# Performance work log

Measured on AMD Instinct MI355X. Metric: run time of the kernel, lower is better.

Reference implementation:

```python
import jax, jax.numpy as jnp
import numpy as np

B, LI, LT = 1, 2048, 256
HID, HEADS, HD = 3072, 24, 128
MLP = 4 * HID  # 12288
EPS = 1e-6


def setup_inputs() -> dict:
    key = jax.random.key(0)
    ks = jax.random.split(key, 12)
    n = lambda k, s, sc=1.0: jax.random.normal(k, s, dtype=jnp.float32) * sc
    # RoPE tables, interleaved-pair layout over head_dim
    theta = 10000.0 ** (-jnp.arange(0, HD, 2, dtype=jnp.float32) / HD)  # [HD/2]
    ang = jnp.arange(LI, dtype=jnp.float32)[:, None] * theta[None, :]   # [LI, HD/2]
    freqs_cos = jnp.repeat(jnp.cos(ang), 2, axis=-1)  # [LI, HD]
    freqs_sin = jnp.repeat(jnp.sin(ang), 2, axis=-1)
    return {
        "img": n(ks[0], (B, LI, HID)),
        "txt": n(ks[1], (B, LT, HID)),
        "vec": n(ks[2], (B, HID)),
        "freqs_cos": freqs_cos,
        "freqs_sin": freqs_sin,
        "w1": n(ks[3], (3 * HID + MLP, HID), 0.02),
        "b1": jnp.zeros((3 * HID + MLP,), jnp.float32),
        "w2": n(ks[4], (HID, HID + MLP), 0.02),
        "b2": jnp.zeros((HID,), jnp.float32),
        "q_norm_w": jnp.ones((HD,), jnp.float32),
        "k_norm_w": jnp.ones((HD,), jnp.float32),
        "mod_w": n(ks[5], (3 * HID, HID), 0.02),
        "mod_b": jnp.zeros((3 * HID,), jnp.float32),
        "txt_len": LT,
    }


def _layernorm(x):  # no affine, eps=1e-6
    mu = x.mean(-1, keepdims=True)
    var = ((x - mu) ** 2).mean(-1, keepdims=True)
    return (x - mu) * jax.lax.rsqrt(var + EPS)


def _rmsnorm(x, w):  # per-head-dim RMSNorm with affine weight
    ms = (x * x).mean(-1, keepdims=True)
    return x * jax.lax.rsqrt(ms + EPS) * w


def _rope(x, cos, sin):  # x: [B,L,H,D]; interleaved complex rotation
    xr = x.reshape(*x.shape[:-1], HD // 2, 2)
    rot = jnp.stack([-xr[..., 1], xr[..., 0]], axis=-1).reshape(x.shape)
    return x * cos[None, :, None, :] + rot * sin[None, :, None, :]


def reference(img, txt, vec, freqs_cos, freqs_sin, w1, b1, w2, b2,
              q_norm_w, k_norm_w, mod_w, mod_b, txt_len):
    H = img.shape[-1]
    Li = img.shape[1]
    # modulation: SiLU(vec) @ W -> shift, scale, gate
    mod = jax.nn.silu(vec) @ mod_w.T + mod_b           # [B, 3H]
    shift, scale, gate = jnp.split(mod, 3, axis=-1)
    modulate = lambda x: x * (1.0 + scale[:, None, :]) + shift[:, None, :]
    img_mod = modulate(_layernorm(img))
    txt_mod = modulate(_layernorm(txt))
    x_mod = jnp.concatenate([img_mod, txt_mod], axis=1)  # [B,S,H]
    Bb, S = x_mod.shape[0], x_mod.shape[1]
    # fused QKV projection (slices of linear1)
    qkv = x_mod @ w1[: 3 * H].T + b1[: 3 * H]
    q, k, v = [t.reshape(Bb, S, HEADS, HD) for t in jnp.split(qkv, 3, axis=-1)]
    q = _rmsnorm(q, q_norm_w)
    k = _rmsnorm(k, k_norm_w)
    # RoPE only on the img portion of the sequence
    q = jnp.concatenate([_rope(q[:, :Li], freqs_cos, freqs_sin), q[:, Li:]], axis=1)
    k = jnp.concatenate([_rope(k[:, :Li], freqs_cos, freqs_sin), k[:, Li:]], axis=1)
    # full (non-causal) attention over img+txt tokens
    logits = jnp.einsum('bqhd,bkhd->bhqk', q, k) * (HD ** -0.5)
    probs = jax.nn.softmax(logits, axis=-1)
    attn = jnp.einsum('bhqk,bkhd->bqhd', probs, v).reshape(Bb, S, H)
    # MLP branch (linear1 mlp slice) with gelu-tanh, then fused linear2
    mlp = jax.nn.gelu(x_mod @ w1[3 * H:].T + b1[3 * H:], approximate=True)
    out = jnp.concatenate([attn, mlp], axis=-1) @ w2.T + b2  # [B,S,H]
    img_out = img + gate[:, None, :] * out[:, :-txt_len]
    txt_out = txt + gate[:, None, :] * out[:, -txt_len:]
    return img_out, txt_out
```

## Files before the change

kernel.cpp:

```cpp
#include <hip/hip_runtime.h>
#include <hip/hip_bf16.h>

#define DI __device__ __forceinline__

typedef __attribute__((ext_vector_type(8))) short bf8;
typedef __attribute__((ext_vector_type(4))) float f4;
typedef __attribute__((ext_vector_type(8))) unsigned short us8;

#define LI    2048
#define LT    256
#define SEQ   2304
#define HID   3072
#define NHEAD 24
#define HD    128
#define N1    21504
#define QKVW  9216
#define N2CAT 15360

DI unsigned short f2bf(float f) {
  union { float f; unsigned u; } v; v.f = f;
  unsigned r = v.u + 0x7FFFu + ((v.u >> 16) & 1u);
  return (unsigned short)(r >> 16);
}
DI float bf2f(unsigned short h) {
  union { unsigned u; float f; } v; v.u = ((unsigned)h) << 16;
  return v.f;
}

DI void gload16(const void* g, void* l) {
  __builtin_amdgcn_global_load_lds(
      (const __attribute__((address_space(1))) void*)g,
      (__attribute__((address_space(3))) void*)l, 16, 0, 0);
}

DI f4 mfma16(bf8 a, bf8 b, f4 c) {
  return __builtin_amdgcn_mfma_f32_16x16x32_bf16(a, b, c, 0, 0, 0);
}

__global__ void k_mod(const float* __restrict__ vec, const float* __restrict__ mw,
                      const float* __restrict__ mb, float* __restrict__ mod) {
  int row = blockIdx.x * 4 + (threadIdx.x >> 6);
  int lane = threadIdx.x & 63;
  const float4* wr = (const float4*)(mw + (size_t)row * HID);
  const float4* vv = (const float4*)vec;
  float s = 0.f;
  for (int i = lane; i < HID / 4; i += 64) {
    float4 w4 = wr[i], x4 = vv[i];
    s += (x4.x / (1.f + __expf(-x4.x))) * w4.x;
    s += (x4.y / (1.f + __expf(-x4.y))) * w4.y;
    s += (x4.z / (1.f + __expf(-x4.z))) * w4.z;
    s += (x4.w / (1.f + __expf(-x4.w))) * w4.w;
  }
#pragma unroll
  for (int m = 32; m; m >>= 1) s += __shfl_xor(s, m);
  if (lane == 0) mod[row] = s + mb[row];
}

__global__ void k_lnmod(const float* __restrict__ img, const float* __restrict__ txt,
                        const float* __restrict__ mod, unsigned short* __restrict__ xmod) {
  int t = blockIdx.x;
  const float* x = (t < LI) ? (img + (size_t)t * HID) : (txt + (size_t)(t - LI) * HID);
  const float4* x4 = (const float4*)x;
  float4 v[3];
  float s = 0.f, ss = 0.f;
#pragma unroll
  for (int j = 0; j < 3; ++j) {
    v[j] = x4[threadIdx.x + j * 256];
    s  += v[j].x + v[j].y + v[j].z + v[j].w;
    ss += v[j].x * v[j].x + v[j].y * v[j].y + v[j].z * v[j].z + v[j].w * v[j].w;
  }
#pragma unroll
  for (int m = 32; m; m >>= 1) { s += __shfl_xor(s, m); ss += __shfl_xor(ss, m); }
  __shared__ float red[8];
  int wv = threadIdx.x >> 6;
  if ((threadIdx.x & 63) == 0) { red[wv] = s; red[4 + wv] = ss; }
  __syncthreads();
  s = red[0] + red[1] + red[2] + red[3];
  ss = red[4] + red[5] + red[6] + red[7];
  float mu = s * (1.f / HID);
  float var = ss * (1.f / HID) - mu * mu;
  float inv = rsqrtf(var + 1e-6f);
  const float* shift = mod;
  const float* scale = mod + HID;
#pragma unroll
  for (int j = 0; j < 3; ++j) {
    int i = threadIdx.x + j * 256;
    int c = i * 4;
    ushort4 o;
    o.x = f2bf((v[j].x - mu) * inv * (1.f + scale[c + 0]) + shift[c + 0]);
    o.y = f2bf((v[j].y - mu) * inv * (1.f + scale[c + 1]) + shift[c + 1]);
    o.z = f2bf((v[j].z - mu) * inv * (1.f + scale[c + 2]) + shift[c + 2]);
    o.w = f2bf((v[j].w - mu) * inv * (1.f + scale[c + 3]) + shift[c + 3]);
    ((ushort4*)xmod)[(size_t)t * (HID / 4) + i] = o;
  }
}

__global__ void k_f2bf(const float* __restrict__ in, unsigned short* __restrict__ out, int n4) {
  int stride = gridDim.x * blockDim.x;
  for (int i = blockIdx.x * blockDim.x + threadIdx.x; i < n4; i += stride) {
    float4 f = ((const float4*)in)[i];
    ushort4 o;
    o.x = f2bf(f.x); o.y = f2bf(f.y); o.z = f2bf(f.z); o.w = f2bf(f.w);
    ((ushort4*)out)[i] = o;
  }
}

#define BAR()    asm volatile("s_barrier" ::: "memory")
#define VMCNT6() asm volatile("s_waitcnt vmcnt(6)" ::: "memory")
#define LGKM0()  do { asm volatile("s_waitcnt lgkmcnt(0)" ::: "memory"); \
                      __builtin_amdgcn_sched_barrier(0); } while (0)

__global__ __launch_bounds__(512, 2) void k_gemm1(const unsigned short* __restrict__ xmod,
    const unsigned short* __restrict__ w1b, const float* __restrict__ b1,
    unsigned short* __restrict__ qkv, unsigned short* __restrict__ amlp) {
  __shared__ unsigned short As[2][256 * 64];
  __shared__ unsigned short Bs[2][256 * 64];
  const int K = HID;
  const int NT = K / 64;
  int tid = threadIdx.x, lane = tid & 63, wid = tid >> 6;
  int wr = wid >> 2, wc = wid & 3;

  int b = blockIdx.x;
  const int Q = 756 / 8, R = 756 % 8;
  int xcd = b & 7, idx = b >> 3;
  int wg = (xcd < R ? xcd * (Q + 1) : R * (Q + 1) + (xcd - R) * Q) + idx;
  int bm = wg % 9, bn = wg / 9;

  const unsigned short* Ag = xmod + (size_t)bm * 256 * K;
  const unsigned short* Bg = w1b + (size_t)bn * 256 * K;

  int sgran = (lane & 7) ^ ((lane >> 3) & 7);
  int srow = wid * 16 + (lane >> 3);

#define STAGE_A(bufi, t, hh) do { \
    gload16(Ag + (size_t)((hh)*128 + srow) * K + (t)*64 + sgran*8, \
            &As[bufi][((hh)*128 + wid*16) * 64]); \
    gload16(Ag + (size_t)((hh)*128 + 8 + srow) * K + (t)*64 + sgran*8, \
            &As[bufi][((hh)*128 + wid*16 + 8) * 64]); \
  } while (0)
#define STAGE_B(bufi, t, hh) do { \
    gload16(Bg + (size_t)((hh)*128 + srow) * K + (t)*64 + sgran*8, \
            &Bs[bufi][((hh)*128 + wid*16) * 64]); \
    gload16(Bg + (size_t)((hh)*128 + 8 + srow) * K + (t)*64 + sgran*8, \
            &Bs[bufi][((hh)*128 + wid*16 + 8) * 64]); \
  } while (0)

  int rA = wr * 128 + (lane & 15);
  int rB = wc * 64 + (lane & 15);
  int qq = lane >> 4, l7 = lane & 7;

  f4 acc[8][4];
#pragma unroll
  for (int m = 0; m < 8; ++m)
#pragma unroll
    for (int n = 0; n < 4; ++n) acc[m][n] = (f4){0.f, 0.f, 0.f, 0.f};
  bf8 a[8][2], bfr[4][2];

#define LOADFRAGS(bufi) do { \
    _Pragma("unroll") for (int m = 0; m < 8; ++m) \
      _Pragma("unroll") for (int s = 0; s < 2; ++s) \
        a[m][s] = *(const bf8*)&As[bufi][(rA + m*16)*64 + (((s*4 + qq) ^ l7) << 3)]; \
    _Pragma("unroll") for (int n = 0; n < 4; ++n) \
      _Pragma("unroll") for (int s = 0; s < 2; ++s) \
        bfr[n][s] = *(const bf8*)&Bs[bufi][(rB + n*16)*64 + (((s*4 + qq) ^ l7) << 3)]; \
  } while (0)

#define QUAD(mh, nh) do { \
    __builtin_amdgcn_s_setprio(1); \
    _Pragma("unroll") for (int m = 4*(mh); m < 4*(mh)+4; ++m) \
      _Pragma("unroll") for (int n = 2*(nh); n < 2*(nh)+2; ++n) \
        _Pragma("unroll") for (int s = 0; s < 2; ++s) \
          acc[m][n] = mfma16(a[m][s], bfr[n][s], acc[m][n]); \
    __builtin_amdgcn_s_setprio(0); \
  } while (0)

  STAGE_A(0, 0, 0); STAGE_A(0, 0, 1); STAGE_B(0, 0, 0); STAGE_B(0, 0, 1);
  STAGE_A(1, 1, 0); STAGE_A(1, 1, 1); STAGE_B(1, 1, 0);
  VMCNT6();
  BAR();

  for (int i = 0; i < NT / 2; ++i) {
    int t1 = 2 * i + 1;
    int t2 = 2 * i + 2; if (t2 > NT - 1) t2 = NT - 1;
    int t3 = 2 * i + 3; if (t3 > NT - 1) t3 = NT - 1;
    LOADFRAGS(0);
    STAGE_B(1, t1, 1);
    LGKM0();
    QUAD(0, 0);
    BAR();
    STAGE_A(0, t2, 0); QUAD(0, 1);
    STAGE_A(0, t2, 1); QUAD(1, 0);
    STAGE_B(0, t2, 0); QUAD(1, 1);
    VMCNT6();
    BAR();
    LOADFRAGS(1);
    STAGE_B(0, t2, 1);
    LGKM0();
    QUAD(0, 0);
    BAR();
    STAGE_A(1, t3, 0); QUAD(0, 1);
    STAGE_A(1, t3, 1); QUAD(1, 0);
    STAGE_B(1, t3, 0); QUAD(1, 1);
    VMCNT6();
    BAR();
  }

  int r0 = bm * 256 + wr * 128 + ((lane >> 4) << 2);
  int c0 = bn * 256 + wc * 64 + (lane & 15);
  bool isqkv = (bn * 256) < QKVW;
#pragma unroll
  for (int m = 0; m < 8; ++m) {
#pragma unroll
    for (int n = 0; n < 4; ++n) {
      int col = c0 + n * 16;
      float bias = b1[col];
#pragma unroll
      for (int j = 0; j < 4; ++j) {
        int row = r0 + m * 16 + j;
        float v = acc[m][n][j] + bias;
        if (isqkv) {
          qkv[(size_t)row * QKVW + col] = f2bf(v);
        } else {
          float u = 0.7978845608f * (v + 0.044715f * v * v * v);
          float g = v / (1.f + __expf(-2.f * u));
          amlp[(size_t)row * N2CAT + (col - 6144)] = f2bf(g);
        }
      }
    }
  }
#undef STAGE_A
#undef STAGE_B
#undef LOADFRAGS
#undef QUAD
}

DI void gemm_core(const unsigned short* __restrict__ A, const unsigned short* __restrict__ Bw,
                  int K, int bm, int bn, unsigned short* As, unsigned short* Bs, f4 acc[4][4]) {
  int tid = threadIdx.x;
  int lane = tid & 63;
  int wr = (tid >> 7) & 1;
  int wc = (tid >> 6) & 1;
#pragma unroll
  for (int m = 0; m < 4; ++m)
#pragma unroll
    for (int n = 0; n < 4; ++n) acc[m][n] = (f4){0.f, 0.f, 0.f, 0.f};

  int rbase = tid >> 3;
  int slg = (tid & 7) ^ (rbase & 7);
  const unsigned short* Ag = A + (size_t)(bm * 128 + rbase) * K + slg * 8;
  const unsigned short* Bg = Bw + (size_t)(bn * 128 + rbase) * K + slg * 8;
  unsigned short* Asd = As + tid * 8;
  unsigned short* Bsd = Bs + tid * 8;

  int rA = wr * 64 + (lane & 15);
  int rB = wc * 64 + (lane & 15);
  int cb = (lane >> 4) * 8;
  int cx = (lane & 7) << 3;

  for (int k0 = 0; k0 < K; k0 += 64) {
    __syncthreads();
#pragma unroll
    for (int j = 0; j < 4; ++j) {
      gload16(Ag + (size_t)(j * 32) * K + k0, Asd + j * 2048);
      gload16(Bg + (size_t)(j * 32) * K + k0, Bsd + j * 2048);
    }
    __syncthreads();
#pragma unroll
    for (int kk = 0; kk < 2; ++kk) {
      bf8 av[4], bv[4];
#pragma unroll
      for (int m = 0; m < 4; ++m)
        av[m] = *(const bf8*)&As[(rA + m * 16) * 64 + ((kk * 32 + cb) ^ cx)];
#pragma unroll
      for (int n = 0; n < 4; ++n)
        bv[n] = *(const bf8*)&Bs[(rB + n * 16) * 64 + ((kk * 32 + cb) ^ cx)];
#pragma unroll
      for (int m = 0; m < 4; ++m)
#pragma unroll
        for (int n = 0; n < 4; ++n)
          acc[m][n] = mfma16(av[m], bv[n], acc[m][n]);
    }
  }
}

__global__ __launch_bounds__(256) void k_gemm2(const unsigned short* __restrict__ amlp,
    const unsigned short* __restrict__ w2b, const float* __restrict__ b2,
    const float* __restrict__ img, const float* __restrict__ txt,
    const float* __restrict__ gate, float* __restrict__ out) {
  __shared__ unsigned short As[128 * 64], Bs[128 * 64];
  int nb = gridDim.x;
  int b = blockIdx.x;
  int bsw = (b & 7) * (nb >> 3) + (b >> 3);
  int bm = bsw % 18, bn = bsw / 18;
  f4 acc[4][4];
  gemm_core(amlp, w2b, N2CAT, bm, bn, As, Bs, acc);
  int lane = threadIdx.x & 63;
  int wr = (threadIdx.x >> 7) & 1, wc = (threadIdx.x >> 6) & 1;
  int r0 = bm * 128 + wr * 64 + ((lane >> 4) << 2);
  int c0 = bn * 128 + wc * 64 + (lane & 15);
#pragma unroll
  for (int m = 0; m < 4; ++m) {
#pragma unroll
    for (int n = 0; n < 4; ++n) {
      int col = c0 + n * 16;
      float bias = b2[col];
      float gt = gate[col];
#pragma unroll
      for (int j = 0; j < 4; ++j) {
        int row = r0 + m * 16 + j;
        float v = acc[m][n][j] + bias;
        float res = (row < LI) ? img[(size_t)row * HID + col]
                               : txt[(size_t)(row - LI) * HID + col];
        out[(size_t)row * HID + col] = res + gt * v;
      }
    }
  }
}

__global__ void k_qknorm(unsigned short* __restrict__ qkv, const float* __restrict__ qw,
                         const float* __restrict__ kw, const float* __restrict__ fcos,
                         const float* __restrict__ fsin) {
  int gw = (blockIdx.x * 256 + threadIdx.x) >> 6;
  int lane = threadIdx.x & 63;
  int token = gw / NHEAD, head = gw - token * NHEAD;
  bool dorope = token < LI;
  float c = 1.f, sn = 0.f;
  if (dorope) { c = fcos[token * HD + 2 * lane]; sn = fsin[token * HD + 2 * lane]; }
#pragma unroll
  for (int qk = 0; qk < 2; ++qk) {
    unsigned short* p = qkv + (size_t)token * QKVW + qk * HID + head * HD;
    unsigned u = ((const unsigned*)p)[lane];
    float x0 = bf2f((unsigned short)(u & 0xffff));
    float x1 = bf2f((unsigned short)(u >> 16));
    float ss = x0 * x0 + x1 * x1;
#pragma unroll
    for (int m2 = 32; m2; m2 >>= 1) ss += __shfl_xor(ss, m2);
    float inv = rsqrtf(ss * (1.f / HD) + 1e-6f);
    const float* w = qk ? kw : qw;
    float y0 = x0 * inv * w[2 * lane];
    float y1 = x1 * inv * w[2 * lane + 1];
    if (dorope) { float r0 = y0 * c - y1 * sn; float r1 = y1 * c + y0 * sn; y0 = r0; y1 = r1; }
    ((unsigned*)p)[lane] = ((unsigned)f2bf(y0)) | (((unsigned)f2bf(y1)) << 16);
  }
}

__global__ void k_vt(const unsigned short* __restrict__ qkv, unsigned short* __restrict__ vt) {
  int b = blockIdx.x;
  int h = b / 72; int rem = b - h * 72; int tt = rem >> 1; int dd = rem & 1;
  int t0 = tt * 64, d0 = dd * 64;
  __shared__ unsigned short tile[64 * 65];
  int tid = threadIdx.x;
#pragma unroll
  for (int j = 0; j < 2; ++j) {
    int idx = j * 256 + tid;
    int row = idx >> 3, s = idx & 7;
    us8 vv = *(const us8*)(qkv + (size_t)(t0 + row) * QKVW + 2 * HID + h * HD + d0 + s * 8);
#pragma unroll
    for (int i = 0; i < 8; ++i) tile[row * 65 + s * 8 + i] = vv[i];
  }
  __syncthreads();
#pragma unroll
  for (int j = 0; j < 2; ++j) {
    int idx = j * 256 + tid;
    int dr = idx >> 3, sl = idx & 7;
    us8 o;
#pragma unroll
    for (int i = 0; i < 8; ++i) o[i] = tile[(sl * 8 + i) * 65 + dr];
    *(us8*)(vt + (size_t)(h * HD + d0 + dr) * SEQ + t0 + sl * 8) = o;
  }
}

__global__ __launch_bounds__(256) void k_attn(const unsigned short* __restrict__ qkv,
                                              const unsigned short* __restrict__ vt,
                                              unsigned short* __restrict__ amlp) {
  int b = blockIdx.x;
  int bsw = (b & 7) * 108 + (b >> 3);
  int head = bsw / 36, qt = bsw - head * 36;
  int tid = threadIdx.x, lane = tid & 63, wv = tid >> 6;
  __shared__ unsigned short Qs[64 * 128], Ks[64 * 128], Vs[128 * 64], Ps[64 * 64];
  int qbase = qt * 64;

  {
    int row = tid >> 4, sl = tid & 15;
    int slg = sl ^ (row & 7);
    const unsigned short* qg = qkv + (size_t)(qbase + row) * QKVW + head * HD + slg * 8;
#pragma unroll
    for (int j = 0; j < 4; ++j)
      gload16(qg + (size_t)(j * 16) * QKVW, &Qs[(j * 256 + tid) * 8]);
  }

  float mrun[4], lrun[4];
  f4 oacc[8];
#pragma unroll
  for (int j = 0; j < 4; ++j) { mrun[j] = -1e30f; lrun[j] = 0.f; }
#pragma unroll
  for (int n = 0; n < 8; ++n) oacc[n] = (f4){0.f, 0.f, 0.f, 0.f};
  bf8 qf[4];

  for (int kt = 0; kt < SEQ / 64; ++kt) {
    __syncthreads();
    {
      int rloc = tid >> 4, sl = tid & 15, slg = sl ^ (rloc & 7);
      const unsigned short* kg =
          qkv + HID + (size_t)(kt * 64 + rloc) * QKVW + head * HD + slg * 8;
#pragma unroll
      for (int j = 0; j < 4; ++j) gload16(kg + (size_t)(j * 16) * QKVW, &Ks[(j * 256 + tid) * 8]);
    }
    {
      int rloc = tid >> 3, sl = tid & 7, slg = sl ^ (rloc & 7);
      const unsigned short* vg = vt + (size_t)(head * HD + rloc) * SEQ + kt * 64 + slg * 8;
#pragma unroll
      for (int j = 0; j < 4; ++j) gload16(vg + (size_t)(j * 32) * SEQ, &Vs[(j * 256 + tid) * 8]);
    }
    __syncthreads();
    if (kt == 0) {
#pragma unroll
      for (int kk = 0; kk < 4; ++kk) {
        int row = wv * 16 + (lane & 15);
        int col = (kk * 32 + ((lane >> 4) * 8)) ^ ((lane & 7) << 3);
        qf[kk] = *(const bf8*)&Qs[row * 128 + col];
      }
    }
    f4 sacc[4];
#pragma unroll
    for (int n = 0; n < 4; ++n) sacc[n] = (f4){0.f, 0.f, 0.f, 0.f};
#pragma unroll
    for (int kk = 0; kk < 4; ++kk) {
#pragma unroll
      for (int n = 0; n < 4; ++n) {
        int row = n * 16 + (lane & 15);
        int col = (kk * 32 + ((lane >> 4) * 8)) ^ ((lane & 7) << 3);
        bf8 kf = *(const bf8*)&Ks[row * 128 + col];
        sacc[n] = mfma16(qf[kk], kf, sacc[n]);
      }
    }
    const float SC = 0.08838834764831845f;
    float mj[4];
#pragma unroll
    for (int j = 0; j < 4; ++j)
      mj[j] = fmaxf(fmaxf(sacc[0][j], sacc[1][j]), fmaxf(sacc[2][j], sacc[3][j]));
#pragma unroll
    for (int j = 0; j < 4; ++j) {
#pragma unroll
      for (int mk = 8; mk; mk >>= 1) mj[j] = fmaxf(mj[j], __shfl_xor(mj[j], mk));
    }
    float resc[4], psum[4];
#pragma unroll
    for (int j = 0; j < 4; ++j) {
      float nm = fmaxf(mrun[j], mj[j] * SC);
      resc[j] = __expf(mrun[j] - nm);
      mrun[j] = nm;
      psum[j] = 0.f;
    }
#pragma unroll
    for (int n = 0; n < 4; ++n) {
#pragma unroll
      for (int j = 0; j < 4; ++j) {
        float p = __expf(sacc[n][j] * SC - mrun[j]);
        psum[j] += p;
        int row = wv * 16 + ((lane >> 4) << 2) + j;
        int col = (n * 16 + (lane & 15)) ^ ((row & 7) << 3);
        Ps[row * 64 + col] = f2bf(p);
      }
    }
#pragma unroll
    for (int j = 0; j < 4; ++j) {
#pragma unroll
      for (int mk = 8; mk; mk >>= 1) psum[j] += __shfl_xor(psum[j], mk);
      lrun[j] = lrun[j] * resc[j] + psum[j];
    }
#pragma unroll
    for (int n = 0; n < 8; ++n) {
#pragma unroll
      for (int j = 0; j < 4; ++j) oacc[n][j] *= resc[j];
    }
#pragma unroll
    for (int kk = 0; kk < 2; ++kk) {
      int prow = wv * 16 + (lane & 15);
      int pcol = (kk * 32 + ((lane >> 4) * 8)) ^ ((lane & 7) << 3);
      bf8 pa = *(const bf8*)&Ps[prow * 64 + pcol];
#pragma unroll
      for (int n = 0; n < 8; ++n) {
        int vrow = n * 16 + (lane & 15);
        int vcol = (kk * 32 + ((lane >> 4) * 8)) ^ ((vrow & 7) << 3);
        bf8 vf = *(const bf8*)&Vs[vrow * 64 + vcol];
        oacc[n] = mfma16(pa, vf, oacc[n]);
      }
    }
  }
#pragma unroll
  for (int j = 0; j < 4; ++j) {
    float invl = 1.f / lrun[j];
    int row = qbase + wv * 16 + ((lane >> 4) << 2) + j;
#pragma unroll
    for (int n = 0; n < 8; ++n) {
      int col = head * HD + n * 16 + (lane & 15);
      amlp[(size_t)row * N2CAT + col] = f2bf(oacc[n][j] * invl);
    }
  }
}

extern "C" void kernel_launch(void* const* d_in, const int* in_sizes, int n_in,
                              void* d_out, int out_size, void* d_ws, size_t ws_size,
                              hipStream_t stream) {
  (void)in_sizes; (void)n_in; (void)out_size; (void)ws_size;
  const float* img  = (const float*)d_in[0];
  const float* txt  = (const float*)d_in[1];
  const float* vec  = (const float*)d_in[2];
  const float* fcos = (const float*)d_in[3];
  const float* fsin = (const float*)d_in[4];
  const float* w1   = (const float*)d_in[5];
  const float* b1   = (const float*)d_in[6];
  const float* w2   = (const float*)d_in[7];
  const float* b2   = (const float*)d_in[8];
  const float* qnw  = (const float*)d_in[9];
  const float* knw  = (const float*)d_in[10];
  const float* mw   = (const float*)d_in[11];
  const float* mb   = (const float*)d_in[12];
  float* out = (float*)d_out;

  char* ws = (char*)d_ws;
  float*          mod  = (float*)(ws);
  unsigned short* xmod = (unsigned short*)(ws + 40960);
  unsigned short* w1b  = (unsigned short*)(ws + 14196736);
  unsigned short* qkv  = (unsigned short*)(ws + 146317312);
  unsigned short* amlp = (unsigned short*)(ws + 188784640);
  unsigned short* vtb  = xmod;
  unsigned short* w2b  = w1b;

  k_mod<<<QKVW / 4, 256, 0, stream>>>(vec, mw, mb, mod);
  k_lnmod<<<SEQ, 256, 0, stream>>>(img, txt, mod, xmod);
  k_f2bf<<<2048, 256, 0, stream>>>(w1, w1b, N1 * HID / 4);
  k_gemm1<<<756, 512, 0, stream>>>(xmod, w1b, b1, qkv, amlp);
  k_qknorm<<<SEQ * NHEAD / 4, 256, 0, stream>>>(qkv, qnw, knw, fcos, fsin);
  k_vt<<<NHEAD * 36 * 2, 256, 0, stream>>>(qkv, vtb);
  k_f2bf<<<2048, 256, 0, stream>>>(w2, w2b, HID * N2CAT / 4);
  k_attn<<<864, 256, 0, stream>>>(qkv, vtb, amlp);
  k_gemm2<<<18 * 24, 256, 0, stream>>>(amlp, w2b, b2, img, txt, mod + 2 * HID, out);
}
```

Measured before the change: 1.031 ms.

## Restructure GEMM1 main loop into fine-grained interleaved LDS-read/MFMA/prefetch groups

Replaces the bulk fragment load followed by four MFMA quadrants with a schedule that reads A/B fragments per quadrant (split into low/high halves). Each quadrant's LDS reads, global prefetch of the next tile half, and MFMA block are separated by barriers. The aim is to cut register pressure from holding all fragments and to overlap LDS reads and global loads with MFMA work more evenly. It changes the vmcnt wait depth and adds more barriers per tile, which may add synchronisation stalls.

```diff
diff --git a/kernel.cpp b/kernel.cpp
--- a/kernel.cpp
+++ b/kernel.cpp
@@ -106,7 +106,8 @@
 }
 
 #define BAR()    asm volatile("s_barrier" ::: "memory")
-#define VMCNT6() asm volatile("s_waitcnt vmcnt(6)" ::: "memory")
+#define VMCNT2() asm volatile("s_waitcnt vmcnt(2)" ::: "memory")
+#define VMCNT0() asm volatile("s_waitcnt vmcnt(0)" ::: "memory")
 #define LGKM0()  do { asm volatile("s_waitcnt lgkmcnt(0)" ::: "memory"); \
                       __builtin_amdgcn_sched_barrier(0); } while (0)
 
@@ -154,56 +155,74 @@
   for (int m = 0; m < 8; ++m)
 #pragma unroll
     for (int n = 0; n < 4; ++n) acc[m][n] = (f4){0.f, 0.f, 0.f, 0.f};
-  bf8 a[8][2], bfr[4][2];
-
-#define LOADFRAGS(bufi) do { \
-    _Pragma("unroll") for (int m = 0; m < 8; ++m) \
-      _Pragma("unroll") for (int s = 0; s < 2; ++s) \
-        a[m][s] = *(const bf8*)&As[bufi][(rA + m*16)*64 + (((s*4 + qq) ^ l7) << 3)]; \
-    _Pragma("unroll") for (int n = 0; n < 4; ++n) \
-      _Pragma("unroll") for (int s = 0; s < 2; ++s) \
-        bfr[n][s] = *(const bf8*)&Bs[bufi][(rB + n*16)*64 + (((s*4 + qq) ^ l7) << 3)]; \
+  bf8 aL[4][2], aH[4][2], bL[2][2], bH[2][2];
+
+#define RD(buf, r, s) (*(const bf8*)&buf[(r) * 64 + ((((s)*4 + qq) ^ l7) << 3)])
+
+#define GROUP(C, tt, tn, tn2) do { \
+     \
+    _Pragma("unroll") for (int m = 0; m < 4; ++m) \
+      _Pragma("unroll") for (int s = 0; s < 2; ++s) aL[m][s] = RD(As[C], rA + m*16, s); \
+    _Pragma("unroll") for (int n = 0; n < 2; ++n) \
+      _Pragma("unroll") for (int s = 0; s < 2; ++s) bL[n][s] = RD(Bs[C], rB + n*16, s); \
+    STAGE_A(1-(C), tn, 1); \
+    LGKM0(); \
+    __builtin_amdgcn_s_setprio(1); \
+    _Pragma("unroll") for (int m = 0; m < 4; ++m) \
+      _Pragma("unroll") for (int n = 0; n < 2; ++n) \
+        _Pragma("unroll") for (int s = 0; s < 2; ++s) \
+          acc[m][n] = mfma16(aL[m][s], bL[n][s], acc[m][n]); \
+    __builtin_amdgcn_s_setprio(0); \
+    BAR(); \
+     \
+    _Pragma("unroll") for (int n = 0; n < 2; ++n) \
+      _Pragma("unroll") for (int s = 0; s < 2; ++s) bH[n][s] = RD(Bs[C], rB + (n+2)*16, s); \
+    STAGE_B(1-(C), tn, 0); \
+    LGKM0(); \
+    __builtin_amdgcn_s_setprio(1); \
+    _Pragma("unroll") for (int m = 0; m < 4; ++m) \
+      _Pragma("unroll") for (int n = 0; n < 2; ++n) \
+        _Pragma("unroll") for (int s = 0; s < 2; ++s) \
+          acc[m][n+2] = mfma16(aL[m][s], bH[n][s], acc[m][n+2]); \
+    __builtin_amdgcn_s_setprio(0); \
+    BAR(); \
+     \
+    _Pragma("unroll") for (int m = 0; m < 4; ++m) \
+      _Pragma("unroll") for (int s = 0; s < 2; ++s) aH[m][s] = RD(As[C], rA + (m+4)*16, s); \
+    STAGE_B(1-(C), tn, 1); \
+    LGKM0(); \
+    __builtin_amdgcn_s_setprio(1); \
+    _Pragma("unroll") for (int m = 0; m < 4; ++m) \
+      _Pragma("unroll") for (int n = 0; n < 2; ++n) \
+        _Pragma("unroll") for (int s = 0; s < 2; ++s) \
+          acc[m+4][n+2] = mfma16(aH[m][s], bH[n][s], acc[m+4][n+2]); \
+    __builtin_amdgcn_s_setprio(0); \
+    BAR(); \
+     \
+    STAGE_A(C, tn2, 0); \
+    __builtin_amdgcn_s_setprio(1); \
+    _Pragma("unroll") for (int m = 0; m < 4; ++m) \
+      _Pragma("unroll") for (int n = 0; n < 2; ++n) \
+        _Pragma("unroll") for (int s = 0; s < 2; ++s) \
+          acc[m+4][n] = mfma16(aH[m][s], bL[n][s], acc[m+4][n]); \
+    __builtin_amdgcn_s_setprio(0); \
+    VMCNT2();    \
+    BAR(); \
   } while (0)
 
-#define QUAD(mh, nh) do { \
-    __builtin_amdgcn_s_setprio(1); \
-    _Pragma("unroll") for (int m = 4*(mh); m < 4*(mh)+4; ++m) \
-      _Pragma("unroll") for (int n = 2*(nh); n < 2*(nh)+2; ++n) \
-        _Pragma("unroll") for (int s = 0; s < 2; ++s) \
-          acc[m][n] = mfma16(a[m][s], bfr[n][s], acc[m][n]); \
-    __builtin_amdgcn_s_setprio(0); \
-  } while (0)
-
   STAGE_A(0, 0, 0); STAGE_A(0, 0, 1); STAGE_B(0, 0, 0); STAGE_B(0, 0, 1);
-  STAGE_A(1, 1, 0); STAGE_A(1, 1, 1); STAGE_B(1, 1, 0);
-  VMCNT6();
+  STAGE_A(1, 1, 0);
+  VMCNT2();
   BAR();
 
   for (int i = 0; i < NT / 2; ++i) {
-    int t1 = 2 * i + 1;
-    int t2 = 2 * i + 2; if (t2 > NT - 1) t2 = NT - 1;
-    int t3 = 2 * i + 3; if (t3 > NT - 1) t3 = NT - 1;
-    LOADFRAGS(0);
-    STAGE_B(1, t1, 1);
-    LGKM0();
-    QUAD(0, 0);
-    BAR();
-    STAGE_A(0, t2, 0); QUAD(0, 1);
-    STAGE_A(0, t2, 1); QUAD(1, 0);
-    STAGE_B(0, t2, 0); QUAD(1, 1);
-    VMCNT6();
-    BAR();
-    LOADFRAGS(1);
-    STAGE_B(0, t2, 1);
-    LGKM0();
-    QUAD(0, 0);
-    BAR();
-    STAGE_A(1, t3, 0); QUAD(0, 1);
-    STAGE_A(1, t3, 1); QUAD(1, 0);
-    STAGE_B(1, t3, 0); QUAD(1, 1);
-    VMCNT6();
-    BAR();
-  }
+    int t0 = 2 * i, t1 = 2 * i + 1;
+    int n1 = t0 + 2; if (n1 > NT - 1) n1 = NT - 1;
+    int n2 = t0 + 3; if (n2 > NT - 1) n2 = NT - 1;
+    GROUP(0, t0, t0 + 1, n1);
+    GROUP(1, t1, n1, n2);
+  }
+  VMCNT0();
 
   int r0 = bm * 256 + wr * 128 + ((lane >> 4) << 2);
   int c0 = bn * 256 + wc * 64 + (lane & 15);
@@ -230,8 +249,8 @@
   }
 #undef STAGE_A
 #undef STAGE_B
-#undef LOADFRAGS
-#undef QUAD
+#undef RD
+#undef GROUP
 }
 
 DI void gemm_core(const unsigned short* __restrict__ A, const unsigned short* __restrict__ Bw,
```

Result: faster. 983.8 us (-4.6%).
